# Optimization experiments

Hardware: AMD Instinct MI355X
Metric: run time of the kernel (lower is better)

The kernel has to match this reference:

```python
import jax, jax.numpy as jnp
import numpy as np

B, L, N, HS, HD, C = 4, 200, 160, 768, 256, 16  # batch, bert len, word len, bert hidden, dense hidden, classes


def setup_inputs() -> dict:
    key = jax.random.key(0)
    ks = jax.random.split(key, 8)
    transformer_out = jax.random.normal(ks[0], (B, L + 1, HS), dtype=jnp.float32)
    word_mapback = jnp.sort(jax.random.randint(ks[1], (B, L), 0, N), axis=-1)
    token_length = jnp.maximum(jax.random.randint(ks[2], (B,), 0, N), N // 2)
    length = jnp.maximum(jax.random.randint(ks[3], (B,), 0, L), 3 * L // 4)
    Wd = jax.random.normal(ks[4], (HS, HD), dtype=jnp.float32) * 0.02
    bd = jnp.zeros((HD,), dtype=jnp.float32)
    Wc = jax.random.normal(ks[5], (3 * HD, C), dtype=jnp.float32) * 0.02
    bc = jnp.zeros((C,), dtype=jnp.float32)
    return dict(transformer_out=transformer_out, Wd=Wd, bd=bd, Wc=Wc, bc=bc,
                word_mapback=word_mapback, token_length=token_length, length=length)


def reference(transformer_out, Wd, bd, Wc, bc, word_mapback, token_length, length):
    # mask over bert positions (after dropping CLS at index 0)
    bert_indi = (jnp.arange(L) < length[:, None]).astype(jnp.float32)[..., None]   # [B,L,1]
    h = transformer_out[:, 1:L + 1, :] * bert_indi                                  # [B,L,HS]
    onehot = jax.nn.one_hot(word_mapback, N, dtype=jnp.float32) * bert_indi         # [B,L,N]
    dense_h = h @ Wd + bd                                                           # [B,L,HD]
    # word-piece -> word mean pooling (one-hot bmm + count normalize)
    pooled = jnp.einsum('bln,blh->bnh', onehot, dense_h)                             # [B,N,HD]
    wnt = onehot.sum(axis=1)                                                         # [B,N]
    pooled = pooled / jnp.where(wnt == 0, 1.0, wnt)[..., None]
    # candidate (i,j) upper-triangular valid-span mask
    tok_mask = (jnp.arange(N) < token_length[:, None]).astype(jnp.float32)           # [B,N]
    cand = jnp.triu(jnp.ones((N, N), jnp.float32))[None] * (tok_mask[:, None, :] * tok_mask[:, :, None])  # [B,N,N]
    # boundary features: [start_repr ; end_repr]
    boundary = jnp.concatenate([
        jnp.broadcast_to(pooled[:, :, None, :], (B, N, N, HD)),
        jnp.broadcast_to(pooled[:, None, :, :], (B, N, N, HD))], axis=-1) * cand[..., None]
    # span sums: span[b,i,k,d] = sum_{i<=j<=k} pooled[b,j,d]*tok_mask[b,j], via prefix sums
    pv = jnp.cumsum(pooled * tok_mask[..., None], axis=1)                            # P[k]
    pv0 = jnp.concatenate([jnp.zeros((B, 1, HD), pv.dtype), pv[:, :-1]], axis=1)     # P[i-1]
    span = (pv[:, None, :, :] - pv0[:, :, None, :]) * cand[..., None]                # [B,N,N,HD]
    # span averaging: divide by span length (k - i + 1), clamped to 1 elsewhere
    diff = jnp.arange(1, N + 1)[None, :] - jnp.arange(N)[:, None]                    # diff[i,k] = k+1-i
    span = span / jnp.where(diff > 0, diff, 1).astype(jnp.float32)[None, :, :, None]
    table = jnp.concatenate([boundary, span], axis=-1)                               # [B,N,N,3*HD]
    logits = (table @ Wc + bc) * cand[..., None]                                     # [B,N,N,C]
    return logits
```

## Files before the change

kernel.cpp:

```cpp
#include <hip/hip_runtime.h>

#define B 4
#define L 200
#define N 160
#define HS 768
#define HD 256
#define C 16

#define KP 784
#define WJ 48
#define KS 4
#define KSL (KP / KS)
#define NROW (B * N)

__global__ __launch_bounds__(256) void prep_kernel(
    const float* __restrict__ TO,
    const float* __restrict__ Wd,
    const float* __restrict__ bd,
    const float* __restrict__ Wc,
    const int*   __restrict__ wm,
    const int*   __restrict__ lengths,
    float* __restrict__ hs_s,
    float* __restrict__ Wfull)
{
    const int blk = blockIdx.x;
    const int t = threadIdx.x;

    if (blk < NROW) {
        const int row = blk;
        const int b = row / N, n = row % N;
        const int len = lengths[b];
        const int* map = wm + b * L;

        int lo = 0, hi = L;
        while (lo < hi) { int m = (lo + hi) >> 1; if (map[m] < n) lo = m + 1; else hi = m; }
        int lo2 = lo, hi2 = L;
        while (lo2 < hi2) { int m = (lo2 + hi2) >> 1; if (map[m] < n + 1) lo2 = m + 1; else hi2 = m; }
        const int start = lo < len ? lo : len;
        const int stop  = lo2 < len ? lo2 : len;
        const int cnt   = stop - start;
        const float ci  = (cnt > 0) ? 1.0f / (float)cnt : 0.0f;

        float a0 = 0.f, a1 = 0.f, a2 = 0.f;
        const float* base = TO + ((size_t)b * (L + 1) + 1) * HS;
        for (int l = start; l < stop; ++l) {
            const float* r = base + (size_t)l * HS;
            a0 += r[t]; a1 += r[t + 256]; a2 += r[t + 512];
        }
        float* hr = hs_s + (size_t)row * KP;
        hr[t] = a0 * ci; hr[t + 256] = a1 * ci; hr[t + 512] = a2 * ci;
        if (t < 16) hr[768 + t] = (t == 0 && cnt > 0) ? 1.0f : 0.0f;
    } else {
        __shared__ float wc[3 * HD * C];
        for (int e = t; e < 3 * HD * C; e += 256) wc[e] = Wc[e];
        __syncthreads();

        const int wb = blk - NROW;
        const int kl = t >> 4, c = t & 15;
        if (wb < 48) {
            const int k = wb * 16 + kl;
            const float4* wd4 = (const float4*)(Wd + (size_t)k * HD);
            float acc0 = 0.f, acc1 = 0.f, acc2 = 0.f;
            #pragma unroll 8
            for (int q = 0; q < HD / 4; ++q) {
                const float4 w = wd4[q];
                const int d = 4 * q;
                acc0 += w.x * wc[(d) * C + c]              + w.y * wc[(d + 1) * C + c]
                      + w.z * wc[(d + 2) * C + c]          + w.w * wc[(d + 3) * C + c];
                acc1 += w.x * wc[(HD + d) * C + c]         + w.y * wc[(HD + d + 1) * C + c]
                      + w.z * wc[(HD + d + 2) * C + c]     + w.w * wc[(HD + d + 3) * C + c];
                acc2 += w.x * wc[(2 * HD + d) * C + c]     + w.y * wc[(2 * HD + d + 1) * C + c]
                      + w.z * wc[(2 * HD + d + 2) * C + c] + w.w * wc[(2 * HD + d + 3) * C + c];
            }
            float* wr = Wfull + (size_t)k * WJ;
            wr[c] = acc0; wr[16 + c] = acc1; wr[32 + c] = acc2;
        } else {
            if (t < WJ) {
                const int m = t >> 4, cc = t & 15;
                const float4* bd4 = (const float4*)bd;
                float acc = 0.f;
                #pragma unroll 8
                for (int q = 0; q < HD / 4; ++q) {
                    const float4 w = bd4[q];
                    const int d = 4 * q;
                    acc += w.x * wc[(m * HD + d) * C + cc]     + w.y * wc[(m * HD + d + 1) * C + cc]
                         + w.z * wc[(m * HD + d + 2) * C + cc] + w.w * wc[(m * HD + d + 3) * C + cc];
                }
                Wfull[(size_t)768 * WJ + t] = acc;
            }
            for (int idx = t; idx < 15 * WJ; idx += 256)
                Wfull[(size_t)769 * WJ + idx] = 0.f;
        }
    }
}

__global__ __launch_bounds__(192) void gemm_kernel(
    const float* __restrict__ hs_s,
    const float* __restrict__ Wfull,
    const int*   __restrict__ token_length,
    float* __restrict__ part)
{
    const int t  = threadIdx.x;
    const int tj = t % WJ;
    const int tr = t / WJ;
    const int row = blockIdx.y * 4 + tr;
    const int k0  = blockIdx.x * KSL;

    const float* in = hs_s + (size_t)row * KP + k0;
    const float* wf = Wfull + (size_t)k0 * WJ + tj;

    float acc = 0.f;
    #pragma unroll 7
    for (int q = 0; q < KSL / 4; ++q) {
        const float4 v = *(const float4*)(in + 4 * q);
        acc += v.x * wf[(size_t)(4 * q) * WJ]     + v.y * wf[(size_t)(4 * q + 1) * WJ]
             + v.z * wf[(size_t)(4 * q + 2) * WJ] + v.w * wf[(size_t)(4 * q + 3) * WJ];
    }
    const int b = row / N, n = row % N;
    if (tj >= 32 && n >= token_length[b]) acc = 0.f;
    part[((size_t)blockIdx.x * NROW + row) * WJ + tj] = acc;
}

__global__ __launch_bounds__(256) void finalize_kernel(
    const float* __restrict__ part,
    const float* __restrict__ bc,
    const int*   __restrict__ token_length,
    float4* __restrict__ out)
{
    const int it = blockIdx.x;
    const int b  = blockIdx.y;
    const int t  = threadIdx.x;
    const int tl = token_length[b];

    __shared__ float sBT[N * 32];
    __shared__ float sA[8 * 16];
    __shared__ float sS[(N + 1) * 16];
    __shared__ float pref[16 * 16];

    for (int e = t; e < N * 32; e += 256) {
        const int n = e >> 5, j2 = e & 31;
        const size_t base = ((size_t)b * N + n) * WJ + 16 + j2;
        sBT[e] = part[base]
               + part[(size_t)1 * NROW * WJ + base]
               + part[(size_t)2 * NROW * WJ + base]
               + part[(size_t)3 * NROW * WJ + base];
    }
    if (t < 128) {
        const int il = t >> 4, c = t & 15;
        const size_t base = ((size_t)b * N + it * 8 + il) * WJ + c;
        sA[t] = part[base]
              + part[(size_t)1 * NROW * WJ + base]
              + part[(size_t)2 * NROW * WJ + base]
              + part[(size_t)3 * NROW * WJ + base];
    }
    if (t < 16) sS[t] = 0.f;
    __syncthreads();

    const int c = t & 15, g = t >> 4;
    {
        float run = 0.f;
        const int nb = g * 10;
        for (int u = 0; u < 10; ++u) {
            run += sBT[(nb + u) * 32 + 16 + c];
            sS[(nb + u + 1) * 16 + c] = run;
        }
        pref[g * 16 + c] = run;
    }
    __syncthreads();
    if (t < 16) {
        float off = 0.f;
        for (int g2 = 0; g2 < 16; ++g2) {
            const float tmp = pref[g2 * 16 + t];
            pref[g2 * 16 + t] = off;
            off += tmp;
        }
    }
    __syncthreads();
    {
        const float off = pref[g * 16 + c];
        const int nb = g * 10;
        for (int u = 0; u < 10; ++u) sS[(nb + u + 1) * 16 + c] += off;
    }
    __syncthreads();

    for (int q = 0; q < 20; ++q) {
        const int qid = t + q * 256;
        const int cq  = qid & 3;
        const int k   = (qid >> 2) % N;
        const int il  = (qid >> 2) / N;
        const int i   = it * 8 + il;

        float4 v = {0.f, 0.f, 0.f, 0.f};
        if ((i <= k) & (i < tl) & (k < tl)) {
            const float4 a   = *(const float4*)&sA[il * 16 + cq * 4];
            const float4 bb  = *(const float4*)&sBT[k * 32 + cq * 4];
            const float4 sk  = *(const float4*)&sS[(k + 1) * 16 + cq * 4];
            const float4 si  = *(const float4*)&sS[i * 16 + cq * 4];
            const float4 bcq = *(const float4*)&bc[cq * 4];
            const float inv = 1.0f / (float)(k - i + 1);
            v.x = a.x + bb.x + (sk.x - si.x) * inv + bcq.x;
            v.y = a.y + bb.y + (sk.y - si.y) * inv + bcq.y;
            v.z = a.z + bb.z + (sk.z - si.z) * inv + bcq.z;
            v.w = a.w + bb.w + (sk.w - si.w) * inv + bcq.w;
        }
        out[((size_t)(b * N + i) * N + k) * 4 + cq] = v;
    }
}

extern "C" void kernel_launch(void* const* d_in, const int* in_sizes, int n_in,
                              void* d_out, int out_size, void* d_ws, size_t ws_size,
                              hipStream_t stream) {
    const float* TO   = (const float*)d_in[0];
    const float* Wd   = (const float*)d_in[1];
    const float* bd   = (const float*)d_in[2];
    const float* Wc   = (const float*)d_in[3];
    const float* bc   = (const float*)d_in[4];
    const int*   wm   = (const int*)d_in[5];
    const int*   tokl = (const int*)d_in[6];
    const int*   len  = (const int*)d_in[7];

    float* ws    = (float*)d_ws;
    float* hs_s  = ws;
    float* Wfull = hs_s + (size_t)NROW * KP;
    float* part  = Wfull + (size_t)KP * WJ;

    prep_kernel<<<NROW + 49, 256, 0, stream>>>(TO, Wd, bd, Wc, wm, len, hs_s, Wfull);
    gemm_kernel<<<dim3(KS, NROW / 4), 192, 0, stream>>>(hs_s, Wfull, tokl, part);
    finalize_kernel<<<dim3(20, B), 256, 0, stream>>>(part, bc, tokl, (float4*)d_out);
}
```

Measured before the change: 35.69 us.

## Fuse three kernels into one persistent kernel with grid barriers

Merges the prep, GEMM and finalize kernels into a single 256-block persistent kernel separated by atomic-counter grid barriers. Each block loops over several prep tasks. The folded weight matrix is stored transposed and staged in shared memory for the GEMM phase. The aim is to cut the launch gaps between kernels, at the cost of a memset, spin-wait barriers that assume all 256 blocks are co-resident, and fewer blocks doing the work in each phase.

```diff
diff --git a/kernel.cpp b/kernel.cpp
--- a/kernel.cpp
+++ b/kernel.cpp
@@ -12,198 +12,240 @@
 #define KS 4
 #define KSL (KP / KS)
 #define NROW (B * N)
-
-__global__ __launch_bounds__(256) void prep_kernel(
+#define NBLK 256
+#define NTHR 256
+
+__device__ __forceinline__ void grid_barrier(unsigned* bar, int idx) {
+    __syncthreads();
+    if (threadIdx.x == 0) {
+        __threadfence();
+        atomicAdd(&bar[idx * 32], 1u);
+        while (__hip_atomic_load(&bar[idx * 32], __ATOMIC_ACQUIRE,
+                                 __HIP_MEMORY_SCOPE_AGENT) < (unsigned)NBLK) {
+            __builtin_amdgcn_s_sleep(1);
+        }
+        __threadfence();
+    }
+    __syncthreads();
+}
+
+__global__ __launch_bounds__(NTHR) void mega_kernel(
     const float* __restrict__ TO,
     const float* __restrict__ Wd,
     const float* __restrict__ bd,
     const float* __restrict__ Wc,
+    const float* __restrict__ bc,
     const int*   __restrict__ wm,
-    const int*   __restrict__ lengths,
+    const int*   __restrict__ tokl,
+    const int*   __restrict__ len,
+    unsigned* bar,
     float* __restrict__ hs_s,
-    float* __restrict__ Wfull)
+    float* __restrict__ WfT,
+    float* __restrict__ part,
+    float4* __restrict__ out)
 {
     const int blk = blockIdx.x;
-    const int t = threadIdx.x;
-
-    if (blk < NROW) {
-        const int row = blk;
-        const int b = row / N, n = row % N;
-        const int len = lengths[b];
-        const int* map = wm + b * L;
-
-        int lo = 0, hi = L;
-        while (lo < hi) { int m = (lo + hi) >> 1; if (map[m] < n) lo = m + 1; else hi = m; }
-        int lo2 = lo, hi2 = L;
-        while (lo2 < hi2) { int m = (lo2 + hi2) >> 1; if (map[m] < n + 1) lo2 = m + 1; else hi2 = m; }
-        const int start = lo < len ? lo : len;
-        const int stop  = lo2 < len ? lo2 : len;
-        const int cnt   = stop - start;
-        const float ci  = (cnt > 0) ? 1.0f / (float)cnt : 0.0f;
-
-        float a0 = 0.f, a1 = 0.f, a2 = 0.f;
-        const float* base = TO + ((size_t)b * (L + 1) + 1) * HS;
-        for (int l = start; l < stop; ++l) {
-            const float* r = base + (size_t)l * HS;
-            a0 += r[t]; a1 += r[t + 256]; a2 += r[t + 512];
-        }
-        float* hr = hs_s + (size_t)row * KP;
-        hr[t] = a0 * ci; hr[t + 256] = a1 * ci; hr[t + 512] = a2 * ci;
-        if (t < 16) hr[768 + t] = (t == 0 && cnt > 0) ? 1.0f : 0.0f;
-    } else {
-        __shared__ float wc[3 * HD * C];
-        for (int e = t; e < 3 * HD * C; e += 256) wc[e] = Wc[e];
-        __syncthreads();
-
-        const int wb = blk - NROW;
-        const int kl = t >> 4, c = t & 15;
-        if (wb < 48) {
-            const int k = wb * 16 + kl;
-            const float4* wd4 = (const float4*)(Wd + (size_t)k * HD);
-            float acc0 = 0.f, acc1 = 0.f, acc2 = 0.f;
-            #pragma unroll 8
-            for (int q = 0; q < HD / 4; ++q) {
-                const float4 w = wd4[q];
-                const int d = 4 * q;
-                acc0 += w.x * wc[(d) * C + c]              + w.y * wc[(d + 1) * C + c]
-                      + w.z * wc[(d + 2) * C + c]          + w.w * wc[(d + 3) * C + c];
-                acc1 += w.x * wc[(HD + d) * C + c]         + w.y * wc[(HD + d + 1) * C + c]
-                      + w.z * wc[(HD + d + 2) * C + c]     + w.w * wc[(HD + d + 3) * C + c];
-                acc2 += w.x * wc[(2 * HD + d) * C + c]     + w.y * wc[(2 * HD + d + 1) * C + c]
-                      + w.z * wc[(2 * HD + d + 2) * C + c] + w.w * wc[(2 * HD + d + 3) * C + c];
-            }
-            float* wr = Wfull + (size_t)k * WJ;
-            wr[c] = acc0; wr[16 + c] = acc1; wr[32 + c] = acc2;
-        } else {
-            if (t < WJ) {
-                const int m = t >> 4, cc = t & 15;
-                const float4* bd4 = (const float4*)bd;
-                float acc = 0.f;
+    const int t   = threadIdx.x;
+
+    __shared__ float sbuf[12288];
+    __shared__ int   s_wm[B * L];
+    __shared__ int   s_len[B], s_tok[B];
+    __shared__ int   s_ss[3 * 2];
+    __shared__ float s_ci[3];
+
+    for (int e = t; e < B * L; e += NTHR) s_wm[e] = wm[e];
+    if (t < B) { s_len[t] = len[t]; s_tok[t] = tokl[t]; }
+    __syncthreads();
+
+    if (t < 3) {
+        const int task = blk + NBLK * t;
+        if (task < NROW) {
+            const int b = task / N, n = task % N;
+            const int ln = s_len[b];
+            const int* map = s_wm + b * L;
+            int lo = 0, hi = L;
+            while (lo < hi) { int m = (lo + hi) >> 1; if (map[m] < n) lo = m + 1; else hi = m; }
+            int lo2 = lo, hi2 = L;
+            while (lo2 < hi2) { int m = (lo2 + hi2) >> 1; if (map[m] < n + 1) lo2 = m + 1; else hi2 = m; }
+            const int start = lo < ln ? lo : ln;
+            const int stop  = lo2 < ln ? lo2 : ln;
+            s_ss[t * 2] = start; s_ss[t * 2 + 1] = stop;
+            s_ci[t] = (stop > start) ? 1.0f / (float)(stop - start) : 0.0f;
+        }
+    }
+    __syncthreads();
+
+    for (int ti = 0; ti < 3; ++ti) {
+        const int task = blk + NBLK * ti;
+        if (task < NROW) {
+            const int start = s_ss[ti * 2], stop = s_ss[ti * 2 + 1];
+            const float ci = s_ci[ti];
+            const int b = task / N;
+            float a0 = 0.f, a1 = 0.f, a2 = 0.f;
+            const float* base = TO + ((size_t)b * (L + 1) + 1) * HS;
+            for (int l = start; l < stop; ++l) {
+                const float* r = base + (size_t)l * HS;
+                a0 += r[t]; a1 += r[t + 256]; a2 += r[t + 512];
+            }
+            float* hr = hs_s + (size_t)task * KP;
+            hr[t] = a0 * ci; hr[t + 256] = a1 * ci; hr[t + 512] = a2 * ci;
+            if (t < 16) hr[768 + t] = (t == 0 && ci > 0.f) ? 1.0f : 0.0f;
+        } else if (task < NROW + 49) {
+            const int wb = task - NROW;
+            __syncthreads();
+            for (int e = t; e < 3 * HD * C; e += NTHR) sbuf[e] = Wc[e];
+            __syncthreads();
+            const int kl = t >> 4, c = t & 15;
+            if (wb < 48) {
+                const int k = wb * 16 + kl;
+                const float4* wd4 = (const float4*)(Wd + (size_t)k * HD);
+                float acc0 = 0.f, acc1 = 0.f, acc2 = 0.f;
                 #pragma unroll 8
                 for (int q = 0; q < HD / 4; ++q) {
-                    const float4 w = bd4[q];
+                    const float4 w = wd4[q];
                     const int d = 4 * q;
-                    acc += w.x * wc[(m * HD + d) * C + cc]     + w.y * wc[(m * HD + d + 1) * C + cc]
-                         + w.z * wc[(m * HD + d + 2) * C + cc] + w.w * wc[(m * HD + d + 3) * C + cc];
+                    acc0 += w.x * sbuf[d * C + c]              + w.y * sbuf[(d + 1) * C + c]
+                          + w.z * sbuf[(d + 2) * C + c]        + w.w * sbuf[(d + 3) * C + c];
+                    acc1 += w.x * sbuf[(HD + d) * C + c]       + w.y * sbuf[(HD + d + 1) * C + c]
+                          + w.z * sbuf[(HD + d + 2) * C + c]   + w.w * sbuf[(HD + d + 3) * C + c];
+                    acc2 += w.x * sbuf[(2*HD + d) * C + c]     + w.y * sbuf[(2*HD + d + 1) * C + c]
+                          + w.z * sbuf[(2*HD + d + 2) * C + c] + w.w * sbuf[(2*HD + d + 3) * C + c];
                 }
-                Wfull[(size_t)768 * WJ + t] = acc;
-            }
-            for (int idx = t; idx < 15 * WJ; idx += 256)
-                Wfull[(size_t)769 * WJ + idx] = 0.f;
-        }
-    }
-}
-
-__global__ __launch_bounds__(192) void gemm_kernel(
-    const float* __restrict__ hs_s,
-    const float* __restrict__ Wfull,
-    const int*   __restrict__ token_length,
-    float* __restrict__ part)
-{
-    const int t  = threadIdx.x;
+                WfT[(size_t)c * KP + k]        = acc0;
+                WfT[(size_t)(16 + c) * KP + k] = acc1;
+                WfT[(size_t)(32 + c) * KP + k] = acc2;
+            } else {
+                if (t < WJ) {
+                    const int m = t >> 4, cc = t & 15;
+                    const float4* bd4 = (const float4*)bd;
+                    float acc = 0.f;
+                    #pragma unroll 8
+                    for (int q = 0; q < HD / 4; ++q) {
+                        const float4 w = bd4[q];
+                        const int d = 4 * q;
+                        acc += w.x * sbuf[(m * HD + d) * C + cc]     + w.y * sbuf[(m * HD + d + 1) * C + cc]
+                             + w.z * sbuf[(m * HD + d + 2) * C + cc] + w.w * sbuf[(m * HD + d + 3) * C + cc];
+                    }
+                    WfT[(size_t)t * KP + 768] = acc;
+                }
+                for (int e = t; e < WJ * 15; e += NTHR) {
+                    const int j = e / 15, k = 769 + e % 15;
+                    WfT[(size_t)j * KP + k] = 0.f;
+                }
+            }
+        }
+    }
+
+    grid_barrier(bar, 0);
+
+    const int ks = blk & 3;
+    const int k0 = ks * KSL;
+    for (int e = t; e < WJ * KSL; e += NTHR) {
+        const int j = e / KSL, k = e % KSL;
+        sbuf[j * KSL + k] = WfT[(size_t)j * KP + k0 + k];
+    }
+    __syncthreads();
+
     const int tj = t % WJ;
     const int tr = t / WJ;
-    const int row = blockIdx.y * 4 + tr;
-    const int k0  = blockIdx.x * KSL;
-
-    const float* in = hs_s + (size_t)row * KP + k0;
-    const float* wf = Wfull + (size_t)k0 * WJ + tj;
-
-    float acc = 0.f;
-    #pragma unroll 7
-    for (int q = 0; q < KSL / 4; ++q) {
-        const float4 v = *(const float4*)(in + 4 * q);
-        acc += v.x * wf[(size_t)(4 * q) * WJ]     + v.y * wf[(size_t)(4 * q + 1) * WJ]
-             + v.z * wf[(size_t)(4 * q + 2) * WJ] + v.w * wf[(size_t)(4 * q + 3) * WJ];
-    }
-    const int b = row / N, n = row % N;
-    if (tj >= 32 && n >= token_length[b]) acc = 0.f;
-    part[((size_t)blockIdx.x * NROW + row) * WJ + tj] = acc;
-}
-
-__global__ __launch_bounds__(256) void finalize_kernel(
-    const float* __restrict__ part,
-    const float* __restrict__ bc,
-    const int*   __restrict__ token_length,
-    float4* __restrict__ out)
-{
-    const int it = blockIdx.x;
-    const int b  = blockIdx.y;
-    const int t  = threadIdx.x;
-    const int tl = token_length[b];
-
-    __shared__ float sBT[N * 32];
-    __shared__ float sA[8 * 16];
-    __shared__ float sS[(N + 1) * 16];
-    __shared__ float pref[16 * 16];
-
-    for (int e = t; e < N * 32; e += 256) {
-        const int n = e >> 5, j2 = e & 31;
-        const size_t base = ((size_t)b * N + n) * WJ + 16 + j2;
-        sBT[e] = part[base]
-               + part[(size_t)1 * NROW * WJ + base]
-               + part[(size_t)2 * NROW * WJ + base]
-               + part[(size_t)3 * NROW * WJ + base];
-    }
-    if (t < 128) {
-        const int il = t >> 4, c = t & 15;
-        const size_t base = ((size_t)b * N + it * 8 + il) * WJ + c;
-        sA[t] = part[base]
-              + part[(size_t)1 * NROW * WJ + base]
-              + part[(size_t)2 * NROW * WJ + base]
-              + part[(size_t)3 * NROW * WJ + base];
-    }
-    if (t < 16) sS[t] = 0.f;
-    __syncthreads();
-
-    const int c = t & 15, g = t >> 4;
-    {
-        float run = 0.f;
+    for (int ti = 0; ti < 2; ++ti) {
+        const int task = blk + NBLK * ti;
+        const int rg = task >> 2;
+        if (tr < 5) {
+            const int row = rg * 5 + tr;
+            const float4* in = (const float4*)(hs_s + (size_t)row * KP + k0);
+            const float4* wr = (const float4*)(sbuf + tj * KSL);
+            float acc = 0.f;
+            #pragma unroll 7
+            for (int q = 0; q < KSL / 4; ++q) {
+                const float4 v = in[q];
+                const float4 w = wr[q];
+                acc += v.x * w.x + v.y * w.y + v.z * w.z + v.w * w.w;
+            }
+            const int b = row / N, n = row % N;
+            if (tj >= 32 && n >= s_tok[b]) acc = 0.f;
+            part[((size_t)ks * NROW + row) * WJ + tj] = acc;
+        }
+    }
+
+    grid_barrier(bar, 1);
+
+    if (blk < 80) {
+        const int it = blk % 20;
+        const int b  = blk / 20;
+        const int tl = s_tok[b];
+        float* sBT  = sbuf;
+        float* sA   = sbuf + 5120;
+        float* sS   = sbuf + 5248;
+        float* pref = sbuf + 7824;
+
+        for (int e = t; e < N * 32; e += NTHR) {
+            const int n = e >> 5, j2 = e & 31;
+            const size_t bse = ((size_t)b * N + n) * WJ + 16 + j2;
+            sBT[e] = part[bse]
+                   + part[(size_t)1 * NROW * WJ + bse]
+                   + part[(size_t)2 * NROW * WJ + bse]
+                   + part[(size_t)3 * NROW * WJ + bse];
+        }
+        if (t < 128) {
+            const int il = t >> 4, c = t & 15;
+            const size_t bse = ((size_t)b * N + it * 8 + il) * WJ + c;
+            sA[t] = part[bse]
+                  + part[(size_t)1 * NROW * WJ + bse]
+                  + part[(size_t)2 * NROW * WJ + bse]
+                  + part[(size_t)3 * NROW * WJ + bse];
+        }
+        if (t < 16) sS[t] = 0.f;
+        __syncthreads();
+
+        const int c = t & 15, g = t >> 4;
         const int nb = g * 10;
-        for (int u = 0; u < 10; ++u) {
-            run += sBT[(nb + u) * 32 + 16 + c];
-            sS[(nb + u + 1) * 16 + c] = run;
-        }
-        pref[g * 16 + c] = run;
-    }
-    __syncthreads();
-    if (t < 16) {
-        float off = 0.f;
-        for (int g2 = 0; g2 < 16; ++g2) {
-            const float tmp = pref[g2 * 16 + t];
-            pref[g2 * 16 + t] = off;
-            off += tmp;
-        }
-    }
-    __syncthreads();
-    {
-        const float off = pref[g * 16 + c];
-        const int nb = g * 10;
-        for (int u = 0; u < 10; ++u) sS[(nb + u + 1) * 16 + c] += off;
-    }
-    __syncthreads();
-
-    for (int q = 0; q < 20; ++q) {
-        const int qid = t + q * 256;
-        const int cq  = qid & 3;
-        const int k   = (qid >> 2) % N;
-        const int il  = (qid >> 2) / N;
-        const int i   = it * 8 + il;
-
-        float4 v = {0.f, 0.f, 0.f, 0.f};
-        if ((i <= k) & (i < tl) & (k < tl)) {
-            const float4 a   = *(const float4*)&sA[il * 16 + cq * 4];
-            const float4 bb  = *(const float4*)&sBT[k * 32 + cq * 4];
-            const float4 sk  = *(const float4*)&sS[(k + 1) * 16 + cq * 4];
-            const float4 si  = *(const float4*)&sS[i * 16 + cq * 4];
-            const float4 bcq = *(const float4*)&bc[cq * 4];
-            const float inv = 1.0f / (float)(k - i + 1);
-            v.x = a.x + bb.x + (sk.x - si.x) * inv + bcq.x;
-            v.y = a.y + bb.y + (sk.y - si.y) * inv + bcq.y;
-            v.z = a.z + bb.z + (sk.z - si.z) * inv + bcq.z;
-            v.w = a.w + bb.w + (sk.w - si.w) * inv + bcq.w;
-        }
-        out[((size_t)(b * N + i) * N + k) * 4 + cq] = v;
+        {
+            float run = 0.f;
+            for (int u = 0; u < 10; ++u) {
+                run += sBT[(nb + u) * 32 + 16 + c];
+                sS[(nb + u + 1) * 16 + c] = run;
+            }
+            pref[g * 16 + c] = run;
+        }
+        __syncthreads();
+        if (t < 16) {
+            float off = 0.f;
+            for (int g2 = 0; g2 < 16; ++g2) {
+                const float tmp = pref[g2 * 16 + t];
+                pref[g2 * 16 + t] = off;
+                off += tmp;
+            }
+        }
+        __syncthreads();
+        {
+            const float off = pref[g * 16 + c];
+            for (int u = 0; u < 10; ++u) sS[(nb + u + 1) * 16 + c] += off;
+        }
+        __syncthreads();
+
+        for (int q = 0; q < 20; ++q) {
+            const int qid = t + q * NTHR;
+            const int cq  = qid & 3;
+            const int k   = (qid >> 2) % N;
+            const int il  = (qid >> 2) / N;
+            const int i   = it * 8 + il;
+
+            float4 v = {0.f, 0.f, 0.f, 0.f};
+            if ((i <= k) & (i < tl) & (k < tl)) {
+                const float4 a   = *(const float4*)&sA[il * 16 + cq * 4];
+                const float4 bb  = *(const float4*)&sBT[k * 32 + cq * 4];
+                const float4 sk  = *(const float4*)&sS[(k + 1) * 16 + cq * 4];
+                const float4 si  = *(const float4*)&sS[i * 16 + cq * 4];
+                const float4 bcq = *(const float4*)&bc[cq * 4];
+                const float inv = 1.0f / (float)(k - i + 1);
+                v.x = a.x + bb.x + (sk.x - si.x) * inv + bcq.x;
+                v.y = a.y + bb.y + (sk.y - si.y) * inv + bcq.y;
+                v.z = a.z + bb.z + (sk.z - si.z) * inv + bcq.z;
+                v.w = a.w + bb.w + (sk.w - si.w) * inv + bcq.w;
+            }
+            out[((size_t)(b * N + i) * N + k) * 4 + cq] = v;
+        }
     }
 }
 
@@ -217,14 +259,15 @@
     const float* bc   = (const float*)d_in[4];
     const int*   wm   = (const int*)d_in[5];
     const int*   tokl = (const int*)d_in[6];
-    const int*   len  = (const int*)d_in[7];
-
-    float* ws    = (float*)d_ws;
-    float* hs_s  = ws;
-    float* Wfull = hs_s + (size_t)NROW * KP;
-    float* part  = Wfull + (size_t)KP * WJ;
-
-    prep_kernel<<<NROW + 49, 256, 0, stream>>>(TO, Wd, bd, Wc, wm, len, hs_s, Wfull);
-    gemm_kernel<<<dim3(KS, NROW / 4), 192, 0, stream>>>(hs_s, Wfull, tokl, part);
-    finalize_kernel<<<dim3(20, B), 256, 0, stream>>>(part, bc, tokl, (float4*)d_out);
+    const int*   lenp = (const int*)d_in[7];
+
+    unsigned* bar = (unsigned*)d_ws;
+    float* base   = (float*)d_ws + 64;
+    float* hs_s   = base;
+    float* WfT    = hs_s + (size_t)NROW * KP;
+    float* part   = WfT + (size_t)WJ * KP;
+
+    hipMemsetAsync(bar, 0, 256, stream);
+    mega_kernel<<<NBLK, NTHR, 0, stream>>>(TO, Wd, bd, Wc, bc, wm, tokl, lenp,
+                                           bar, hs_s, WfT, part, (float4*)d_out);
 }
```

After: 100.5 us. 2.82x slower.

## Transpose folded weight matrix and stage it in shared memory for GEMM

Applied to the files above, without the earlier changes.

The folded Wd·Wc weight is now stored transposed (WJ x KP). Its computation is split across three times as many blocks, each using a padded, transposed shared tile of one third of Wc, which shrinks per-block LDS use and gives vectorized dot products. The GEMM kernel stages its weight slice in shared memory so each thread reads float4 rows instead of strided scalar global loads. The word mapback is also cached in shared memory for the binary searches, at the cost of an extra barrier and a staging copy per GEMM block.

```diff
diff --git a/kernel.cpp b/kernel.cpp
--- a/kernel.cpp
+++ b/kernel.cpp
@@ -12,6 +12,7 @@
 #define KS 4
 #define KSL (KP / KS)
 #define NROW (B * N)
+#define WCT_STRIDE 260
 
 __global__ __launch_bounds__(256) void prep_kernel(
     const float* __restrict__ TO,
@@ -21,7 +22,7 @@
     const int*   __restrict__ wm,
     const int*   __restrict__ lengths,
     float* __restrict__ hs_s,
-    float* __restrict__ Wfull)
+    float* __restrict__ WfT)
 {
     const int blk = blockIdx.x;
     const int t = threadIdx.x;
@@ -30,12 +31,15 @@
         const int row = blk;
         const int b = row / N, n = row % N;
         const int len = lengths[b];
-        const int* map = wm + b * L;
+
+        __shared__ int smap[L];
+        for (int e = t; e < L; e += 256) smap[e] = wm[b * L + e];
+        __syncthreads();
 
         int lo = 0, hi = L;
-        while (lo < hi) { int m = (lo + hi) >> 1; if (map[m] < n) lo = m + 1; else hi = m; }
+        while (lo < hi) { int m = (lo + hi) >> 1; if (smap[m] < n) lo = m + 1; else hi = m; }
         int lo2 = lo, hi2 = L;
-        while (lo2 < hi2) { int m = (lo2 + hi2) >> 1; if (map[m] < n + 1) lo2 = m + 1; else hi2 = m; }
+        while (lo2 < hi2) { int m = (lo2 + hi2) >> 1; if (smap[m] < n + 1) lo2 = m + 1; else hi2 = m; }
         const int start = lo < len ? lo : len;
         const int stop  = lo2 < len ? lo2 : len;
         const int cnt   = stop - start;
@@ -50,53 +54,56 @@
         float* hr = hs_s + (size_t)row * KP;
         hr[t] = a0 * ci; hr[t + 256] = a1 * ci; hr[t + 512] = a2 * ci;
         if (t < 16) hr[768 + t] = (t == 0 && cnt > 0) ? 1.0f : 0.0f;
+    } else if (blk < NROW + 147) {
+        const int wb = blk - NROW;
+        const int kb = wb / 3;
+        const int m  = wb % 3;
+
+        __shared__ float wcT[16 * WCT_STRIDE];
+        for (int e = t; e < HD * C; e += 256) {
+            const int d = e >> 4, c = e & 15;
+            wcT[c * WCT_STRIDE + d] = Wc[(size_t)(m * HD + d) * C + c];
+        }
+        __syncthreads();
+
+        const int kl = t >> 4, c = t & 15;
+        const int k = kb * 16 + kl;
+        const float4* wd4 = (const float4*)(Wd + (size_t)k * HD);
+        const float4* wc4 = (const float4*)(wcT + c * WCT_STRIDE);
+        float acc = 0.f;
+        #pragma unroll 8
+        for (int q = 0; q < HD / 4; ++q) {
+            const float4 a = wd4[q];
+            const float4 w = wc4[q];
+            acc += a.x * w.x + a.y * w.y + a.z * w.z + a.w * w.w;
+        }
+        WfT[(size_t)(m * 16 + c) * KP + k] = acc;
     } else {
-        __shared__ float wc[3 * HD * C];
-        for (int e = t; e < 3 * HD * C; e += 256) wc[e] = Wc[e];
-        __syncthreads();
-
-        const int wb = blk - NROW;
-        const int kl = t >> 4, c = t & 15;
-        if (wb < 48) {
-            const int k = wb * 16 + kl;
-            const float4* wd4 = (const float4*)(Wd + (size_t)k * HD);
-            float acc0 = 0.f, acc1 = 0.f, acc2 = 0.f;
+        if (t < WJ) {
+            const int m = t >> 4, c = t & 15;
+            const float4* bd4 = (const float4*)bd;
+            float acc = 0.f;
             #pragma unroll 8
             for (int q = 0; q < HD / 4; ++q) {
-                const float4 w = wd4[q];
+                const float4 w = bd4[q];
                 const int d = 4 * q;
-                acc0 += w.x * wc[(d) * C + c]              + w.y * wc[(d + 1) * C + c]
-                      + w.z * wc[(d + 2) * C + c]          + w.w * wc[(d + 3) * C + c];
-                acc1 += w.x * wc[(HD + d) * C + c]         + w.y * wc[(HD + d + 1) * C + c]
-                      + w.z * wc[(HD + d + 2) * C + c]     + w.w * wc[(HD + d + 3) * C + c];
-                acc2 += w.x * wc[(2 * HD + d) * C + c]     + w.y * wc[(2 * HD + d + 1) * C + c]
-                      + w.z * wc[(2 * HD + d + 2) * C + c] + w.w * wc[(2 * HD + d + 3) * C + c];
+                acc += w.x * Wc[(size_t)(m * HD + d) * C + c]
+                     + w.y * Wc[(size_t)(m * HD + d + 1) * C + c]
+                     + w.z * Wc[(size_t)(m * HD + d + 2) * C + c]
+                     + w.w * Wc[(size_t)(m * HD + d + 3) * C + c];
             }
-            float* wr = Wfull + (size_t)k * WJ;
-            wr[c] = acc0; wr[16 + c] = acc1; wr[32 + c] = acc2;
-        } else {
-            if (t < WJ) {
-                const int m = t >> 4, cc = t & 15;
-                const float4* bd4 = (const float4*)bd;
-                float acc = 0.f;
-                #pragma unroll 8
-                for (int q = 0; q < HD / 4; ++q) {
-                    const float4 w = bd4[q];
-                    const int d = 4 * q;
-                    acc += w.x * wc[(m * HD + d) * C + cc]     + w.y * wc[(m * HD + d + 1) * C + cc]
-                         + w.z * wc[(m * HD + d + 2) * C + cc] + w.w * wc[(m * HD + d + 3) * C + cc];
-                }
-                Wfull[(size_t)768 * WJ + t] = acc;
-            }
-            for (int idx = t; idx < 15 * WJ; idx += 256)
-                Wfull[(size_t)769 * WJ + idx] = 0.f;
+            WfT[(size_t)t * KP + 768] = acc;
+        }
+        for (int e = t; e < WJ * 15; e += 256) {
+            const int j = e / 15, k = 769 + e % 15;
+            WfT[(size_t)j * KP + k] = 0.f;
         }
     }
 }
 
 __global__ __launch_bounds__(192) void gemm_kernel(
     const float* __restrict__ hs_s,
-    const float* __restrict__ Wfull,
+    const float* __restrict__ WfT,
     const int*   __restrict__ token_length,
     float* __restrict__ part)
 {
@@ -106,15 +113,21 @@
     const int row = blockIdx.y * 4 + tr;
     const int k0  = blockIdx.x * KSL;
 
-    const float* in = hs_s + (size_t)row * KP + k0;
-    const float* wf = Wfull + (size_t)k0 * WJ + tj;
-
+    __shared__ float sbuf[WJ * KSL];
+    for (int e = t; e < WJ * KSL; e += 192) {
+        const int j = e / KSL, k = e % KSL;
+        sbuf[j * KSL + k] = WfT[(size_t)j * KP + k0 + k];
+    }
+    __syncthreads();
+
+    const float4* in = (const float4*)(hs_s + (size_t)row * KP + k0);
+    const float4* wr = (const float4*)(sbuf + tj * KSL);
     float acc = 0.f;
     #pragma unroll 7
     for (int q = 0; q < KSL / 4; ++q) {
-        const float4 v = *(const float4*)(in + 4 * q);
-        acc += v.x * wf[(size_t)(4 * q) * WJ]     + v.y * wf[(size_t)(4 * q + 1) * WJ]
-             + v.z * wf[(size_t)(4 * q + 2) * WJ] + v.w * wf[(size_t)(4 * q + 3) * WJ];
+        const float4 v = in[q];
+        const float4 w = wr[q];
+        acc += v.x * w.x + v.y * w.y + v.z * w.z + v.w * w.w;
     }
     const int b = row / N, n = row % N;
     if (tj >= 32 && n >= token_length[b]) acc = 0.f;
@@ -139,27 +152,27 @@
 
     for (int e = t; e < N * 32; e += 256) {
         const int n = e >> 5, j2 = e & 31;
-        const size_t base = ((size_t)b * N + n) * WJ + 16 + j2;
-        sBT[e] = part[base]
-               + part[(size_t)1 * NROW * WJ + base]
-               + part[(size_t)2 * NROW * WJ + base]
-               + part[(size_t)3 * NROW * WJ + base];
+        const size_t bse = ((size_t)b * N + n) * WJ + 16 + j2;
+        sBT[e] = part[bse]
+               + part[(size_t)1 * NROW * WJ + bse]
+               + part[(size_t)2 * NROW * WJ + bse]
+               + part[(size_t)3 * NROW * WJ + bse];
     }
     if (t < 128) {
         const int il = t >> 4, c = t & 15;
-        const size_t base = ((size_t)b * N + it * 8 + il) * WJ + c;
-        sA[t] = part[base]
-              + part[(size_t)1 * NROW * WJ + base]
-              + part[(size_t)2 * NROW * WJ + base]
-              + part[(size_t)3 * NROW * WJ + base];
+        const size_t bse = ((size_t)b * N + it * 8 + il) * WJ + c;
+        sA[t] = part[bse]
+              + part[(size_t)1 * NROW * WJ + bse]
+              + part[(size_t)2 * NROW * WJ + bse]
+              + part[(size_t)3 * NROW * WJ + bse];
     }
     if (t < 16) sS[t] = 0.f;
     __syncthreads();
 
     const int c = t & 15, g = t >> 4;
+    const int nb = g * 10;
     {
         float run = 0.f;
-        const int nb = g * 10;
         for (int u = 0; u < 10; ++u) {
             run += sBT[(nb + u) * 32 + 16 + c];
             sS[(nb + u + 1) * 16 + c] = run;
@@ -178,7 +191,6 @@
     __syncthreads();
     {
         const float off = pref[g * 16 + c];
-        const int nb = g * 10;
         for (int u = 0; u < 10; ++u) sS[(nb + u + 1) * 16 + c] += off;
     }
     __syncthreads();
@@ -217,14 +229,14 @@
     const float* bc   = (const float*)d_in[4];
     const int*   wm   = (const int*)d_in[5];
     const int*   tokl = (const int*)d_in[6];
-    const int*   len  = (const int*)d_in[7];
-
-    float* ws    = (float*)d_ws;
-    float* hs_s  = ws;
-    float* Wfull = hs_s + (size_t)NROW * KP;
-    float* part  = Wfull + (size_t)KP * WJ;
-
-    prep_kernel<<<NROW + 49, 256, 0, stream>>>(TO, Wd, bd, Wc, wm, len, hs_s, Wfull);
-    gemm_kernel<<<dim3(KS, NROW / 4), 192, 0, stream>>>(hs_s, Wfull, tokl, part);
+    const int*   lenp = (const int*)d_in[7];
+
+    float* ws   = (float*)d_ws;
+    float* hs_s = ws;
+    float* WfT  = hs_s + (size_t)NROW * KP;
+    float* part = WfT + (size_t)WJ * KP;
+
+    prep_kernel<<<NROW + 147 + 1, 256, 0, stream>>>(TO, Wd, bd, Wc, wm, lenp, hs_s, WfT);
+    gemm_kernel<<<dim3(KS, NROW / 4), 192, 0, stream>>>(hs_s, WfT, tokl, part);
     finalize_kernel<<<dim3(20, B), 256, 0, stream>>>(part, bc, tokl, (float4*)d_out);
 }
```

Result: faster. 30.85 us (-13.5%).
